# Optimization experiments

Hardware: AMD Instinct MI355X
Metric: run time of the kernel (lower is better)

The kernel has to match this reference:

```python
import jax, jax.numpy as jnp
import numpy as np

B, C, N, D, F = 2048, 64, 64, 64, 128  # batch, cin_hidden, num_features, embed_dim, feature_maps


def setup_inputs() -> dict:
    key = jax.random.key(0)
    k1, k2, k3 = jax.random.split(key, 3)
    xj = jax.random.normal(k1, (B, C, D), dtype=jnp.float32)
    x0 = jax.random.normal(k2, (B, N, D), dtype=jnp.float32)
    # xavier_uniform_ on (F, C, N): fan_in = C*N? torch treats dim1 as fan_in-ish;
    # exact init distribution is irrelevant for correctness testing, use scaled uniform.
    limit = float(np.sqrt(6.0 / (C + N)))
    W = jax.random.uniform(k3, (F, C, N), dtype=jnp.float32, minval=-limit, maxval=limit)
    return {"xj": xj, "x0": x0, "W": W}


def reference(xj, x0, W):
    # Original: hadamard[b,c,n,d] = x0[b,n,d]*xj[b,c,d];
    # out[b,f,c,d] = sum_n hadamard * W[f,c,n]; cin_out = sum_c out; cin_p_out = sum_d cin_out.
    # Fused: cin_out[b,f,d] = sum_{c,n} W[f,c,n] * xj[b,c,d] * x0[b,n,d]
    cin_out = jnp.einsum('bcd,bnd,fcn->bfd', xj, x0, W)  # (B, F, D)
    cin_p_out = jnp.sum(cin_out, axis=-1)  # (B, F)
    return (cin_out, cin_p_out)
```

## Files before the change

### kernel.cpp

```cpp
#include <hip/hip_runtime.h>


typedef _Float16 f16;
typedef __attribute__((ext_vector_type(8))) _Float16 half8;
typedef __attribute__((ext_vector_type(16))) float f32x16;
typedef __attribute__((ext_vector_type(4))) float f32x4;

#define GLOAD16(g, l) __builtin_amdgcn_global_load_lds( \
    (const __attribute__((address_space(1))) void*)(g), \
    (__attribute__((address_space(3))) void*)(l), 16, 0, 0)

__global__ __launch_bounds__(256) void wscat_kernel(const float* __restrict__ W,
                                                    f16* __restrict__ Wb) {
  const int tid = blockIdx.x * 256 + threadIdx.x;
  const int c = tid >> 10, s = tid & 1023;
  const int gk = s >> 6, ln = s & 63;
  const int g = gk >> 2, kk = gk & 3, hi = ln >> 5, lr = ln & 31;
  const int f = g * 32 + lr, n0 = kk * 16 + hi * 8;
  const float* src = W + (size_t)f * 4096 + c * 64 + n0;
  const float4 a = *(const float4*)src;
  const float4 b = *(const float4*)(src + 4);
  half8 r;
  r[0] = (f16)a.x; r[1] = (f16)a.y; r[2] = (f16)a.z; r[3] = (f16)a.w;
  r[4] = (f16)b.x; r[5] = (f16)b.y; r[6] = (f16)b.z; r[7] = (f16)b.w;
  *(half8*)(Wb + (size_t)c * 8192 + s * 8) = r;
}

__global__ __launch_bounds__(512, 2) void cin_kernel(
    const float* __restrict__ xj, const float* __restrict__ x0,
    const f16* __restrict__ Wb, float* __restrict__ out,
    float* __restrict__ pout) {
  __shared__ f16 x0T[4 * 4096];
  __shared__ f16 Wt[4 * 8192];

  const int t = threadIdx.x;
  const int wid = t >> 6, lane = t & 63;
  const int b0 = blockIdx.x * 4;

#pragma unroll
  for (int bb = 0; bb < 4; ++bb) {
    const float* s0 = x0 + (size_t)(b0 + bb) * 4096;
    const int n = lane, d0 = wid * 8;
    const float4 va = *(const float4*)(s0 + n * 64 + d0);
    const float4 vb = *(const float4*)(s0 + n * 64 + d0 + 4);
    const int chb = n >> 3, sub = n & 7;
#pragma unroll
    for (int j = 0; j < 8; ++j) {
      const float v = (j < 4) ? ((const float*)&va)[j] : ((const float*)&vb)[j - 4];
      const int d = d0 + j;
      x0T[bb * 4096 + d * 64 + (((chb) ^ (d & 7)) << 3) + sub] = (f16)v;
    }
  }
  __syncthreads();

  const int wg = wid & 3, bp = wid >> 2;
  const int lr = lane & 31, hi = lane >> 5;

  half8 af[4][4];
#pragma unroll
  for (int mf = 0; mf < 4; ++mf) {
    const int bb = bp * 2 + (mf >> 1);
    const int d = (mf & 1) * 32 + lr;
#pragma unroll
    for (int kk = 0; kk < 4; ++kk)
      af[mf][kk] = *(const half8*)&x0T[bb * 4096 + d * 64 +
                                       (((kk * 2 + hi) ^ (d & 7)) << 3)];
  }

  f32x16 acc[4] = {};

  const f16* wsrc = Wb + ((size_t)wid * 64 + lane) * 8;
  f16* wdst = Wt + ((size_t)wid * 64 + lane) * 8;
  const float* xjp = xj + (size_t)(b0 + bp * 2) * 4096 + lr;

#pragma unroll
  for (int cc = 0; cc < 3; ++cc) {
    GLOAD16(wsrc + (size_t)cc * 8192, wdst + cc * 8192);
    GLOAD16(wsrc + (size_t)cc * 8192 + 4096, wdst + cc * 8192 + 4096);
  }
  float xc0 = xjp[0], xc1 = xjp[32], xc2 = xjp[4096], xc3 = xjp[4096 + 32];

#pragma unroll 1
  for (int c = 0; c < 64; ++c) {
    asm volatile("s_waitcnt vmcnt(8)" ::: "memory");
    __builtin_amdgcn_s_barrier();
    __builtin_amdgcn_sched_barrier(0);

    const f16* wb = Wt + (c & 3) * 8192 + wg * 2048;
    half8 bf0 = *(const half8*)&wb[0 * 512 + lane * 8];
    half8 bf1 = *(const half8*)&wb[1 * 512 + lane * 8];
    half8 bf2 = *(const half8*)&wb[2 * 512 + lane * 8];
    half8 bf3 = *(const half8*)&wb[3 * 512 + lane * 8];

    const int cs = (c < 61) ? c + 3 : 63;
    GLOAD16(wsrc + (size_t)cs * 8192, wdst + ((c + 3) & 3) * 8192);
    GLOAD16(wsrc + (size_t)cs * 8192 + 4096, wdst + ((c + 3) & 3) * 8192 + 4096);

    const int cx = (c < 63) ? c + 1 : 63;
    const float xn0 = xjp[cx * 64], xn1 = xjp[cx * 64 + 32];
    const float xn2 = xjp[4096 + cx * 64], xn3 = xjp[4096 + cx * 64 + 32];

    const f16 xh0 = (f16)xc0, xh1 = (f16)xc1, xh2 = (f16)xc2, xh3 = (f16)xc3;
#pragma unroll
    for (int kk = 0; kk < 4; ++kk) {
      const half8 bfv = (kk == 0) ? bf0 : (kk == 1) ? bf1 : (kk == 2) ? bf2 : bf3;
      acc[0] = __builtin_amdgcn_mfma_f32_32x32x16_f16(af[0][kk] * xh0, bfv, acc[0], 0, 0, 0);
      acc[1] = __builtin_amdgcn_mfma_f32_32x32x16_f16(af[1][kk] * xh1, bfv, acc[1], 0, 0, 0);
      acc[2] = __builtin_amdgcn_mfma_f32_32x32x16_f16(af[2][kk] * xh2, bfv, acc[2], 0, 0, 0);
      acc[3] = __builtin_amdgcn_mfma_f32_32x32x16_f16(af[3][kk] * xh3, bfv, acc[3], 0, 0, 0);
    }
    xc0 = xn0; xc1 = xn1; xc2 = xn2; xc3 = xn3;
  }

  const int fcol = wg * 32 + lr;
  float ps[4];
#pragma unroll
  for (int mf = 0; mf < 4; ++mf) {
    const int b = b0 + bp * 2 + (mf >> 1);
    float* ob = out + (size_t)b * 8192 + (size_t)fcol * 64 + (mf & 1) * 32;
    const f32x16 v = acc[mf];
    float s = 0.f;
#pragma unroll
    for (int q = 0; q < 4; ++q) {
      f32x4 vv = { v[4 * q], v[4 * q + 1], v[4 * q + 2], v[4 * q + 3] };
      *(f32x4*)(ob + q * 8 + hi * 4) = vv;
      s += vv[0] + vv[1] + vv[2] + vv[3];
    }
    ps[mf] = s;
  }
  float pA = ps[0] + ps[1];
  float pB = ps[2] + ps[3];
  pA += __shfl_xor(pA, 32, 64);
  pB += __shfl_xor(pB, 32, 64);
  if (hi == 0) {
    pout[(size_t)(b0 + bp * 2) * 128 + fcol] = pA;
    pout[(size_t)(b0 + bp * 2 + 1) * 128 + fcol] = pB;
  }
}

extern "C" void kernel_launch(void* const* d_in, const int* in_sizes, int n_in,
                              void* d_out, int out_size, void* d_ws, size_t ws_size,
                              hipStream_t stream) {
  const float* xj = (const float*)d_in[0];
  const float* x0 = (const float*)d_in[1];
  const float* W  = (const float*)d_in[2];
  float* out  = (float*)d_out;
  float* pout = out + (size_t)2048 * 128 * 64;
  f16* Wb = (f16*)d_ws;

  wscat_kernel<<<256, 256, 0, stream>>>(W, Wb);
  cin_kernel<<<512, 512, 0, stream>>>(xj, x0, Wb, out, pout);
}
```

Before: 146.1 us.

## Load W fragments directly into registers instead of staging through LDS

Drops the LDS ring buffer, the global_load_lds prefetch and the per-step barriers. Each wave now reads its W fragments straight from global memory into registers, double-buffered across pairs of c steps, and raises MFMA priority with s_setprio. Blocks shrink to 256 threads covering 2 batches, with 1024 blocks launched, so each block no longer shares W staging across 8 waves. This removes barrier stalls and LDS traffic but increases global/L2 reads of W, since every wave now fetches W itself.

Result: slower. 150.9 us (+3.2%).

```diff
diff --git a/kernel.cpp b/kernel.cpp
--- a/kernel.cpp
+++ b/kernel.cpp
@@ -6,9 +6,7 @@
 typedef __attribute__((ext_vector_type(16))) float f32x16;
 typedef __attribute__((ext_vector_type(4))) float f32x4;
 
-#define GLOAD16(g, l) __builtin_amdgcn_global_load_lds( \
-    (const __attribute__((address_space(1))) void*)(g), \
-    (__attribute__((address_space(3))) void*)(l), 16, 0, 0)
+#define MFMA(a, b, c) __builtin_amdgcn_mfma_f32_32x32x16_f16(a, b, c, 0, 0, 0)
 
 __global__ __launch_bounds__(256) void wscat_kernel(const float* __restrict__ W,
                                                     f16* __restrict__ Wb) {
@@ -26,40 +24,41 @@
   *(half8*)(Wb + (size_t)c * 8192 + s * 8) = r;
 }
 
-__global__ __launch_bounds__(512, 2) void cin_kernel(
+__global__ __launch_bounds__(256, 2) void cin_kernel(
     const float* __restrict__ xj, const float* __restrict__ x0,
     const f16* __restrict__ Wb, float* __restrict__ out,
     float* __restrict__ pout) {
-  __shared__ f16 x0T[4 * 4096];
-  __shared__ f16 Wt[4 * 8192];
+  __shared__ f16 x0T[2 * 4096];
 
   const int t = threadIdx.x;
   const int wid = t >> 6, lane = t & 63;
-  const int b0 = blockIdx.x * 4;
+  const int b0 = blockIdx.x * 2;
 
 #pragma unroll
-  for (int bb = 0; bb < 4; ++bb) {
+  for (int bb = 0; bb < 2; ++bb) {
     const float* s0 = x0 + (size_t)(b0 + bb) * 4096;
-    const int n = lane, d0 = wid * 8;
-    const float4 va = *(const float4*)(s0 + n * 64 + d0);
-    const float4 vb = *(const float4*)(s0 + n * 64 + d0 + 4);
+    const int n = lane, d0 = wid * 16;
     const int chb = n >> 3, sub = n & 7;
 #pragma unroll
-    for (int j = 0; j < 8; ++j) {
-      const float v = (j < 4) ? ((const float*)&va)[j] : ((const float*)&vb)[j - 4];
-      const int d = d0 + j;
-      x0T[bb * 4096 + d * 64 + (((chb) ^ (d & 7)) << 3) + sub] = (f16)v;
+    for (int q = 0; q < 4; ++q) {
+      const float4 v = *(const float4*)(s0 + n * 64 + d0 + q * 4);
+#pragma unroll
+      for (int j = 0; j < 4; ++j) {
+        const int d = d0 + q * 4 + j;
+        x0T[bb * 4096 + d * 64 + ((chb ^ (d & 7)) << 3) + sub] =
+            (f16)(((const float*)&v)[j]);
+      }
     }
   }
   __syncthreads();
 
-  const int wg = wid & 3, bp = wid >> 2;
+  const int wg = wid;
   const int lr = lane & 31, hi = lane >> 5;
 
   half8 af[4][4];
 #pragma unroll
   for (int mf = 0; mf < 4; ++mf) {
-    const int bb = bp * 2 + (mf >> 1);
+    const int bb = mf >> 1;
     const int d = (mf & 1) * 32 + lr;
 #pragma unroll
     for (int kk = 0; kk < 4; ++kk)
@@ -69,54 +68,59 @@
 
   f32x16 acc[4] = {};
 
-  const f16* wsrc = Wb + ((size_t)wid * 64 + lane) * 8;
-  f16* wdst = Wt + ((size_t)wid * 64 + lane) * 8;
-  const float* xjp = xj + (size_t)(b0 + bp * 2) * 4096 + lr;
+  const half8* wp = (const half8*)Wb + wg * 256 + lane;
+  const float* xjp = xj + (size_t)b0 * 4096 + lr;
 
-#pragma unroll
-  for (int cc = 0; cc < 3; ++cc) {
-    GLOAD16(wsrc + (size_t)cc * 8192, wdst + cc * 8192);
-    GLOAD16(wsrc + (size_t)cc * 8192 + 4096, wdst + cc * 8192 + 4096);
-  }
-  float xc0 = xjp[0], xc1 = xjp[32], xc2 = xjp[4096], xc3 = xjp[4096 + 32];
+  half8 wA0 = wp[0],        wA1 = wp[64],        wA2 = wp[128],        wA3 = wp[192];
+  half8 wB0 = wp[1024],     wB1 = wp[1024 + 64], wB2 = wp[1024 + 128], wB3 = wp[1024 + 192];
+  float xA0 = xjp[0],   xA1 = xjp[32],   xA2 = xjp[4096],      xA3 = xjp[4128];
+  float xB0 = xjp[64],  xB1 = xjp[96],   xB2 = xjp[4096 + 64], xB3 = xjp[4096 + 96];
 
 #pragma unroll 1
-  for (int c = 0; c < 64; ++c) {
-    asm volatile("s_waitcnt vmcnt(8)" ::: "memory");
-    __builtin_amdgcn_s_barrier();
-    __builtin_amdgcn_sched_barrier(0);
-
-    const f16* wb = Wt + (c & 3) * 8192 + wg * 2048;
-    half8 bf0 = *(const half8*)&wb[0 * 512 + lane * 8];
-    half8 bf1 = *(const half8*)&wb[1 * 512 + lane * 8];
-    half8 bf2 = *(const half8*)&wb[2 * 512 + lane * 8];
-    half8 bf3 = *(const half8*)&wb[3 * 512 + lane * 8];
-
-    const int cs = (c < 61) ? c + 3 : 63;
-    GLOAD16(wsrc + (size_t)cs * 8192, wdst + ((c + 3) & 3) * 8192);
-    GLOAD16(wsrc + (size_t)cs * 8192 + 4096, wdst + ((c + 3) & 3) * 8192 + 4096);
-
-    const int cx = (c < 63) ? c + 1 : 63;
-    const float xn0 = xjp[cx * 64], xn1 = xjp[cx * 64 + 32];
-    const float xn2 = xjp[4096 + cx * 64], xn3 = xjp[4096 + cx * 64 + 32];
-
-    const f16 xh0 = (f16)xc0, xh1 = (f16)xc1, xh2 = (f16)xc2, xh3 = (f16)xc3;
+  for (int cc = 0; cc < 32; ++cc) {
+    {
+      const f16 h0 = (f16)xA0, h1 = (f16)xA1, h2 = (f16)xA2, h3 = (f16)xA3;
+      const int cn = (2 * cc + 2 < 64) ? 2 * cc + 2 : 63;
+      __builtin_amdgcn_s_setprio(1);
 #pragma unroll
-    for (int kk = 0; kk < 4; ++kk) {
-      const half8 bfv = (kk == 0) ? bf0 : (kk == 1) ? bf1 : (kk == 2) ? bf2 : bf3;
-      acc[0] = __builtin_amdgcn_mfma_f32_32x32x16_f16(af[0][kk] * xh0, bfv, acc[0], 0, 0, 0);
-      acc[1] = __builtin_amdgcn_mfma_f32_32x32x16_f16(af[1][kk] * xh1, bfv, acc[1], 0, 0, 0);
-      acc[2] = __builtin_amdgcn_mfma_f32_32x32x16_f16(af[2][kk] * xh2, bfv, acc[2], 0, 0, 0);
-      acc[3] = __builtin_amdgcn_mfma_f32_32x32x16_f16(af[3][kk] * xh3, bfv, acc[3], 0, 0, 0);
+      for (int kk = 0; kk < 4; ++kk) {
+        const half8 w = (kk == 0) ? wA0 : (kk == 1) ? wA1 : (kk == 2) ? wA2 : wA3;
+        acc[0] = MFMA(af[0][kk] * h0, w, acc[0]);
+        acc[1] = MFMA(af[1][kk] * h1, w, acc[1]);
+        acc[2] = MFMA(af[2][kk] * h2, w, acc[2]);
+        acc[3] = MFMA(af[3][kk] * h3, w, acc[3]);
+      }
+      __builtin_amdgcn_s_setprio(0);
+      wA0 = wp[cn * 1024];       wA1 = wp[cn * 1024 + 64];
+      wA2 = wp[cn * 1024 + 128]; wA3 = wp[cn * 1024 + 192];
+      xA0 = xjp[cn * 64];        xA1 = xjp[cn * 64 + 32];
+      xA2 = xjp[cn * 64 + 4096]; xA3 = xjp[cn * 64 + 4128];
     }
-    xc0 = xn0; xc1 = xn1; xc2 = xn2; xc3 = xn3;
+    {
+      const f16 h0 = (f16)xB0, h1 = (f16)xB1, h2 = (f16)xB2, h3 = (f16)xB3;
+      const int cn = (2 * cc + 3 < 64) ? 2 * cc + 3 : 63;
+      __builtin_amdgcn_s_setprio(1);
+#pragma unroll
+      for (int kk = 0; kk < 4; ++kk) {
+        const half8 w = (kk == 0) ? wB0 : (kk == 1) ? wB1 : (kk == 2) ? wB2 : wB3;
+        acc[0] = MFMA(af[0][kk] * h0, w, acc[0]);
+        acc[1] = MFMA(af[1][kk] * h1, w, acc[1]);
+        acc[2] = MFMA(af[2][kk] * h2, w, acc[2]);
+        acc[3] = MFMA(af[3][kk] * h3, w, acc[3]);
+      }
+      __builtin_amdgcn_s_setprio(0);
+      wB0 = wp[cn * 1024];       wB1 = wp[cn * 1024 + 64];
+      wB2 = wp[cn * 1024 + 128]; wB3 = wp[cn * 1024 + 192];
+      xB0 = xjp[cn * 64];        xB1 = xjp[cn * 64 + 32];
+      xB2 = xjp[cn * 64 + 4096]; xB3 = xjp[cn * 64 + 4128];
+    }
   }
 
   const int fcol = wg * 32 + lr;
   float ps[4];
 #pragma unroll
   for (int mf = 0; mf < 4; ++mf) {
-    const int b = b0 + bp * 2 + (mf >> 1);
+    const int b = b0 + (mf >> 1);
     float* ob = out + (size_t)b * 8192 + (size_t)fcol * 64 + (mf & 1) * 32;
     const f32x16 v = acc[mf];
     float s = 0.f;
@@ -133,8 +137,8 @@
   pA += __shfl_xor(pA, 32, 64);
   pB += __shfl_xor(pB, 32, 64);
   if (hi == 0) {
-    pout[(size_t)(b0 + bp * 2) * 128 + fcol] = pA;
-    pout[(size_t)(b0 + bp * 2 + 1) * 128 + fcol] = pB;
+    pout[(size_t)b0 * 128 + fcol] = pA;
+    pout[(size_t)(b0 + 1) * 128 + fcol] = pB;
   }
 }
 
@@ -149,5 +153,5 @@
   f16* Wb = (f16*)d_ws;
 
   wscat_kernel<<<256, 256, 0, stream>>>(W, Wb);
-  cin_kernel<<<512, 512, 0, stream>>>(xj, x0, Wb, out, pout);
+  cin_kernel<<<1024, 256, 0, stream>>>(xj, x0, Wb, out, pout);
 }
```
